# Kernel tuning notes

Hardware: AMD Instinct MI355X
Metric: run time of the kernel (lower is better)

The kernel has to match this reference:

```python
import jax, jax.numpy as jnp
import numpy as np

B, S, F, H, DK = 16, 1024, 512, 8, 64
NEG = 999999.0

def setup_inputs() -> dict:
    key = jax.random.key(0)
    ks = jax.random.split(key, 10)
    s = 1.0 / np.sqrt(F)
    inp = {
        'x': jax.random.normal(ks[0], (B, S, F), dtype=jnp.float32),
        'xlen': jax.random.randint(ks[1], (B,), 1, S + 1, dtype=jnp.int32),
        'WQw': jax.random.uniform(ks[2], (H, DK, F), jnp.float32, -s, s),
        'WQb': jax.random.uniform(ks[3], (H, DK), jnp.float32, -s, s),
        'WKw': jax.random.uniform(ks[4], (H, DK, F), jnp.float32, -s, s),
        'WKb': jax.random.uniform(ks[5], (H, DK), jnp.float32, -s, s),
        'WVw': jax.random.uniform(ks[6], (H, DK, F), jnp.float32, -s, s),
        'WVb': jax.random.uniform(ks[7], (H, DK), jnp.float32, -s, s),
        'WOw': jax.random.uniform(ks[8], (F, H * DK), jnp.float32, -1.0/np.sqrt(H*DK), 1.0/np.sqrt(H*DK)),
        'WOb': jax.random.uniform(ks[9], (F,), jnp.float32, -1.0/np.sqrt(H*DK), 1.0/np.sqrt(H*DK)),
    }
    return inp

def reference(x, xlen, WQw, WQb, WKw, WKb, WVw, WVb, WOw, WOb):
    # batched per-head projections: [B,S,F] x [H,DK,F] -> [B,H,S,DK]
    q = jnp.einsum('bsf,hdf->bhsd', x, WQw) + WQb[None, :, None, :]
    k = jnp.einsum('bsf,hdf->bhsd', x, WKw) + WKb[None, :, None, :]
    v = jnp.einsum('bsf,hdf->bhsd', x, WVw) + WVb[None, :, None, :]
    scores = jnp.einsum('bhsd,bhtd->bhst', q, k) / jnp.sqrt(jnp.float32(DK))
    # additive padding mask; original masks key positions >= xlen[j]-1 (off-by-one preserved)
    key_pos = jnp.arange(S)[None, :]                       # [1,S]
    mask = jnp.where(key_pos >= (xlen - 1)[:, None], -NEG, 0.0).astype(jnp.float32)
    scores = scores + mask[:, None, None, :]               # [B,H,S,S]
    attn = jax.nn.softmax(scores, axis=-1)
    z = jnp.einsum('bhst,bhtd->bhsd', attn, v)             # [B,H,S,DK]
    z = jnp.transpose(z, (0, 2, 1, 3)).reshape(B, S, H * DK)  # concat heads
    return z @ WOw.T + WOb
```

## Files before the change

### kernel.cpp

```cpp
#include <hip/hip_runtime.h>

typedef short bf16x8 __attribute__((ext_vector_type(8)));
typedef float f32x4 __attribute__((ext_vector_type(4)));
typedef unsigned short u16;

#define B_   16
#define S_   1024
#define F_   512
#define H_   8
#define DK_  64


__device__ __forceinline__ u16 f2bf(float f) {
    union { float f; unsigned int u; } v; v.f = f;
    return (u16)((v.u + 0x7FFFu + ((v.u >> 16) & 1u)) >> 16);
}
__device__ __forceinline__ float bf2f(u16 h) {
    union { unsigned int u; float f; } v; v.u = ((unsigned int)h) << 16;
    return v.f;
}
__device__ __forceinline__ bf16x8 cvt8(float4 a, float4 b) {
    union { u16 u[8]; bf16x8 v; } r;
    r.u[0] = f2bf(a.x); r.u[1] = f2bf(a.y); r.u[2] = f2bf(a.z); r.u[3] = f2bf(a.w);
    r.u[4] = f2bf(b.x); r.u[5] = f2bf(b.y); r.u[6] = f2bf(b.z); r.u[7] = f2bf(b.w);
    return r.v;
}

__device__ __forceinline__ void gl_lds16(const u16* g, u16* l) {
    __builtin_amdgcn_global_load_lds(
        (const __attribute__((address_space(1))) unsigned int*)g,
        (__attribute__((address_space(3))) unsigned int*)l,
        16, 0, 0);
}

__global__ __launch_bounds__(256) void cvt_all(
    const float* __restrict__ x,
    const float* __restrict__ wq, const float* __restrict__ wk,
    const float* __restrict__ wv, const float* __restrict__ wo,
    const float* __restrict__ bq, const float* __restrict__ bk,
    const float* __restrict__ bv, const float* __restrict__ bo,
    u16* __restrict__ Xbf, u16* __restrict__ Wbase)
{
    const size_t u = (size_t)blockIdx.x * 256 + threadIdx.x;
    const float* src; u16* dst;
    if (u < 1048576)      { src = x  + u * 8;               dst = Xbf + u * 8; }
    else if (u < 1081344) { src = wq + (u - 1048576) * 8;   dst = Wbase + (u - 1048576) * 8; }
    else if (u < 1114112) { src = wk + (u - 1081344) * 8;   dst = Wbase +  262144 + (u - 1081344) * 8; }
    else if (u < 1146880) { src = wv + (u - 1114112) * 8;   dst = Wbase +  524288 + (u - 1114112) * 8; }
    else if (u < 1179648) { src = wo + (u - 1146880) * 8;   dst = Wbase +  786432 + (u - 1146880) * 8; }
    else if (u < 1179712) { src = bq + (u - 1179648) * 8;   dst = Wbase + 1048576 + (u - 1179648) * 8; }
    else if (u < 1179776) { src = bk + (u - 1179712) * 8;   dst = Wbase + 1049088 + (u - 1179712) * 8; }
    else if (u < 1179840) { src = bv + (u - 1179776) * 8;   dst = Wbase + 1049600 + (u - 1179776) * 8; }
    else                  { src = bo + (u - 1179840) * 8;   dst = Wbase + 1050112 + (u - 1179840) * 8; }
    *(bf16x8*)dst = cvt8(*(const float4*)src, *(const float4*)(src + 4));
}

template <int EPI>
__global__ __launch_bounds__(256) void gemm128(
    const u16* __restrict__ A, const u16* __restrict__ Bm,
    const u16* __restrict__ bias, void* __restrict__ out)
{
    __shared__ __align__(16) u16 AsL[4096];
    __shared__ __align__(16) u16 BsL[4096];

    const int t    = threadIdx.x;
    const int wave = t >> 6, lane = t & 63;
    const int l15  = lane & 15, quad = lane >> 4;
    const int wr   = (wave & 1) * 64, wc = (wave >> 1) * 64;
    const int m0   = blockIdx.x * 128, n0 = blockIdx.y * 128;
    const int sr   = t >> 2, scol = (t & 3) * 8;

    f32x4 acc[4][4];
#pragma unroll
    for (int i = 0; i < 4; i++)
#pragma unroll
        for (int j = 0; j < 4; j++) acc[i][j] = {0.f, 0.f, 0.f, 0.f};

    const u16* Ab = A  + (size_t)(m0 + sr) * 512 + scol;
    const u16* Bb = Bm + (size_t)(n0 + sr) * 512 + scol;
    u16* la = &AsL[t * 8];
    u16* lb = &BsL[t * 8];

    for (int k0 = 0; k0 < 512; k0 += 32) {
        gl_lds16(Ab + k0,         la);
        gl_lds16(Ab + 32768 + k0, la + 2048);
        gl_lds16(Bb + k0,         lb);
        gl_lds16(Bb + 32768 + k0, lb + 2048);
        __syncthreads();
        bf16x8 af[4], bfv[4];
#pragma unroll
        for (int i = 0; i < 4; i++) af[i]  = *(const bf16x8*)&AsL[(wr + i * 16 + l15) * 32 + quad * 8];
#pragma unroll
        for (int j = 0; j < 4; j++) bfv[j] = *(const bf16x8*)&BsL[(wc + j * 16 + l15) * 32 + quad * 8];
#pragma unroll
        for (int i = 0; i < 4; i++)
#pragma unroll
            for (int j = 0; j < 4; j++)
                acc[i][j] = __builtin_amdgcn_mfma_f32_16x16x32_bf16(af[i], bfv[j], acc[i][j], 0, 0, 0);
        __syncthreads();
    }

#pragma unroll
    for (int j = 0; j < 4; j++) {
        const int n  = n0 + wc + j * 16 + l15;
        const float bv = bf2f(bias[n]);
        const int hh = n >> 6, d = n & 63;
#pragma unroll
        for (int i = 0; i < 4; i++) {
#pragma unroll
            for (int r = 0; r < 4; r++) {
                const int m = m0 + wr + i * 16 + quad * 4 + r;
                const float val = acc[i][j][r] + bv;
                if (EPI == 0) {
                    const int b = m >> 10, s = m & 1023;
                    ((u16*)out)[((size_t)(b * 8 + hh) * 1024 + s) * 64 + d] = f2bf(val);
                } else if (EPI == 1) {
                    const int b = m >> 10, s = m & 1023;
                    ((u16*)out)[((size_t)(b * 8 + hh) * 64 + d) * 1024 + s] = f2bf(val);
                } else {
                    ((float*)out)[(size_t)m * 512 + n] = val;
                }
            }
        }
    }
}

__global__ __launch_bounds__(256) void attn(
    const u16* __restrict__ Xbf, const u16* __restrict__ Wqbf,
    const u16* __restrict__ bqbf,
    const u16* __restrict__ Kg, const u16* __restrict__ Vt,
    const int* __restrict__ xlen, u16* __restrict__ Z)
{
    __shared__ __align__(16) u16 smem[13824];

    const int t    = threadIdx.x;
    const int wave = t >> 6, lane = t & 63;
    const int l15  = lane & 15, quad = lane >> 4;
    const int bh   = blockIdx.y, b = bh >> 3, h = bh & 7;
    const int bx   = blockIdx.x;
    const int xm1  = xlen[b] - 1;
    const int wm   = (wave & 1) * 32, wn = (wave >> 1) * 32;

    u16* Ks = smem;
    u16* Vs = smem + 4608;
    u16* PQ = smem + 9216 + wave * 1152;

    f32x4 qa[2][2];
#pragma unroll
    for (int i = 0; i < 2; i++)
#pragma unroll
        for (int j = 0; j < 2; j++) qa[i][j] = {0.f, 0.f, 0.f, 0.f};

    const int sr = t >> 2, scol = (t & 3) * 8;
    const u16* Xb = Xbf  + (size_t)(b * 1024 + bx * 64 + sr) * 512 + scol;
    const u16* Wb = Wqbf + (size_t)(h * 64 + sr) * 512 + scol;
    u16* la = &smem[t * 8];
    u16* lb = &smem[2048 + t * 8];

    for (int k0 = 0; k0 < 512; k0 += 32) {
        gl_lds16(Xb + k0, la);
        gl_lds16(Wb + k0, lb);
        __syncthreads();
        bf16x8 af[2], bfv[2];
#pragma unroll
        for (int i = 0; i < 2; i++) af[i]  = *(const bf16x8*)&smem[(wm + i * 16 + l15) * 32 + quad * 8];
#pragma unroll
        for (int j = 0; j < 2; j++) bfv[j] = *(const bf16x8*)&smem[2048 + (wn + j * 16 + l15) * 32 + quad * 8];
#pragma unroll
        for (int i = 0; i < 2; i++)
#pragma unroll
            for (int j = 0; j < 2; j++)
                qa[i][j] = __builtin_amdgcn_mfma_f32_16x16x32_bf16(af[i], bfv[j], qa[i][j], 0, 0, 0);
        __syncthreads();
    }
#pragma unroll
    for (int j = 0; j < 2; j++) {
        const int d  = wn + j * 16 + l15;
        const float bv = bf2f(bqbf[h * 64 + d]);
#pragma unroll
        for (int i = 0; i < 2; i++) {
#pragma unroll
            for (int r = 0; r < 4; r++) {
                const int row = wm + i * 16 + quad * 4 + r;
                smem[9216 + (row >> 4) * 1152 + (row & 15) * 72 + d] = f2bf((qa[i][j][r] + bv) * 0.125f);
            }
        }
    }
    __syncthreads();

    bf16x8 aq[2];
#pragma unroll
    for (int kk = 0; kk < 2; kk++)
        aq[kk] = *(const bf16x8*)&PQ[l15 * 72 + kk * 32 + quad * 8];

    const size_t baseKV = (size_t)bh * (S_ * DK_);
    const bool domask = (xm1 >= 1);
    const int  Slim   = domask ? xm1 : S_;

    f32x4 o[4];
#pragma unroll
    for (int j = 0; j < 4; j++) o[j] = {0.f, 0.f, 0.f, 0.f};
    float li[4] = {0.f, 0.f, 0.f, 0.f};

    const int srow = t >> 3, scl = (t & 7) * 8;

    for (int t0 = 0; t0 < Slim; t0 += 64) {
        *(uint4*)&Ks[srow * 72 + scl]        = *(const uint4*)&Kg[baseKV + (size_t)(t0 + srow) * 64 + scl];
        *(uint4*)&Ks[(srow + 32) * 72 + scl] = *(const uint4*)&Kg[baseKV + (size_t)(t0 + srow + 32) * 64 + scl];
        *(uint4*)&Vs[srow * 72 + scl]        = *(const uint4*)&Vt[baseKV + (size_t)srow * 1024 + t0 + scl];
        *(uint4*)&Vs[(srow + 32) * 72 + scl] = *(const uint4*)&Vt[baseKV + (size_t)(srow + 32) * 1024 + t0 + scl];
        __syncthreads();

        f32x4 sc[4];
#pragma unroll
        for (int nh = 0; nh < 4; nh++) {
            f32x4 s = {0.f, 0.f, 0.f, 0.f};
#pragma unroll
            for (int kk = 0; kk < 2; kk++) {
                bf16x8 bk = *(const bf16x8*)&Ks[(nh * 16 + l15) * 72 + kk * 32 + quad * 8];
                s = __builtin_amdgcn_mfma_f32_16x16x32_bf16(aq[kk], bk, s, 0, 0, 0);
            }
            sc[nh] = s;
        }
        if (domask && (t0 + 64 > xm1)) {
#pragma unroll
            for (int nh = 0; nh < 4; nh++) {
                const float madd = ((t0 + nh * 16 + l15) >= xm1) ? -999999.0f : 0.0f;
#pragma unroll
                for (int r = 0; r < 4; r++) sc[nh][r] += madd;
            }
        }
#pragma unroll
        for (int r = 0; r < 4; r++) {
            float e0 = __expf(sc[0][r]), e1 = __expf(sc[1][r]);
            float e2 = __expf(sc[2][r]), e3 = __expf(sc[3][r]);
            li[r] += (e0 + e1) + (e2 + e3);
            PQ[(quad * 4 + r) * 72 + l15]      = f2bf(e0);
            PQ[(quad * 4 + r) * 72 + 16 + l15] = f2bf(e1);
            PQ[(quad * 4 + r) * 72 + 32 + l15] = f2bf(e2);
            PQ[(quad * 4 + r) * 72 + 48 + l15] = f2bf(e3);
        }
        bf16x8 ap[2];
#pragma unroll
        for (int kk = 0; kk < 2; kk++)
            ap[kk] = *(const bf16x8*)&PQ[l15 * 72 + kk * 32 + quad * 8];
#pragma unroll
        for (int j = 0; j < 4; j++) {
#pragma unroll
            for (int kk = 0; kk < 2; kk++) {
                bf16x8 bv8 = *(const bf16x8*)&Vs[(j * 16 + l15) * 72 + kk * 32 + quad * 8];
                o[j] = __builtin_amdgcn_mfma_f32_16x16x32_bf16(ap[kk], bv8, o[j], 0, 0, 0);
            }
        }
        __syncthreads();
    }

    float linv[4];
#pragma unroll
    for (int r = 0; r < 4; r++) {
        float rs = li[r];
#pragma unroll
        for (int msk = 1; msk < 16; msk <<= 1) rs += __shfl_xor(rs, msk);
        linv[r] = 1.0f / rs;
    }
#pragma unroll
    for (int j = 0; j < 4; j++) {
#pragma unroll
        for (int r = 0; r < 4; r++) {
            const int s = bx * 64 + wave * 16 + quad * 4 + r;
            Z[((size_t)(b * 1024 + s)) * 512 + h * 64 + j * 16 + l15] = f2bf(o[j][r] * linv[r]);
        }
    }
}

extern "C" void kernel_launch(void* const* d_in, const int* in_sizes, int n_in,
                              void* d_out, int out_size, void* d_ws, size_t ws_size,
                              hipStream_t stream)
{
    (void)in_sizes; (void)n_in; (void)out_size; (void)ws_size;

    const float* x    = (const float*)d_in[0];
    const int*   xlen = (const int*)d_in[1];
    const float* WQw  = (const float*)d_in[2];
    const float* WQb  = (const float*)d_in[3];
    const float* WKw  = (const float*)d_in[4];
    const float* WKb  = (const float*)d_in[5];
    const float* WVw  = (const float*)d_in[6];
    const float* WVb  = (const float*)d_in[7];
    const float* WOw  = (const float*)d_in[8];
    const float* WOb  = (const float*)d_in[9];

    const size_t NQ = (size_t)B_ * H_ * S_ * DK_;
    u16* Kb    = (u16*)d_ws;
    u16* Zb    = Kb + NQ;
    u16* Wbase = Zb + NQ;
    u16* WQbf  = Wbase;
    u16* WKbf  = Wbase + 262144;
    u16* WVbf  = Wbase + 524288;
    u16* WObf  = Wbase + 786432;
    u16* bqbf  = Wbase + 1048576;
    u16* bkbf  = Wbase + 1049088;
    u16* bvbf  = Wbase + 1049600;
    u16* bobf  = Wbase + 1050112;
    u16* Xbf = (u16*)d_out;
    u16* Vb  = Xbf + NQ;

    dim3 blk(256);
    cvt_all<<<dim3(4609), blk, 0, stream>>>(x, WQw, WKw, WVw, WOw,
                                            WQb, WKb, WVb, WOb, Xbf, Wbase);

    dim3 gGemm(128, 4);
    gemm128<0><<<gGemm, blk, 0, stream>>>(Xbf, WKbf, bkbf, Kb);
    gemm128<1><<<gGemm, blk, 0, stream>>>(Xbf, WVbf, bvbf, Vb);

    dim3 gAttn(16, 128);
    attn<<<gAttn, blk, 0, stream>>>(Xbf, WQbf, bqbf, Kb, Vb, xlen, Zb);

    gemm128<2><<<gGemm, blk, 0, stream>>>(Zb, WObf, bobf, d_out);
}
```

Before: 212.4 us.

## Keep attention probabilities in registers by transposing QK^T and permuting K rows

The QK^T MFMA now runs with operands swapped (K as A, Q as B), so each lane holds scores along the key dimension. K rows are stored in LDS with a permutation, which lets the exponentiated scores be packed directly into bf16 A-operand fragments for the PV MFMA. This removes the per-tile LDS write and read of P along with its buffer, and it changes the mask index math and the row-sum reduction to match. The smaller LDS footprint and the launch-bounds hint of 8 blocks aim to raise occupancy, but the register limit may cause spills.

After: 233.9 us. +10.1%, slower.

```diff
diff --git a/kernel.cpp b/kernel.cpp
--- a/kernel.cpp
+++ b/kernel.cpp
@@ -1,4 +1,5 @@
 #include <hip/hip_runtime.h>
+#include <hip/hip_bf16.h>
 
 typedef short bf16x8 __attribute__((ext_vector_type(8)));
 typedef float f32x4 __attribute__((ext_vector_type(4)));
@@ -24,6 +25,11 @@
     r.u[0] = f2bf(a.x); r.u[1] = f2bf(a.y); r.u[2] = f2bf(a.z); r.u[3] = f2bf(a.w);
     r.u[4] = f2bf(b.x); r.u[5] = f2bf(b.y); r.u[6] = f2bf(b.z); r.u[7] = f2bf(b.w);
     return r.v;
+}
+__device__ __forceinline__ unsigned int pk2(float lo, float hi) {
+    union { __hip_bfloat162 h; unsigned int u; } c;
+    c.h = __float22bfloat162_rn(make_float2(lo, hi));
+    return c.u;
 }
 
 __device__ __forceinline__ void gl_lds16(const u16* g, u16* l) {
@@ -125,13 +131,13 @@
     }
 }
 
-__global__ __launch_bounds__(256) void attn(
+__global__ __launch_bounds__(256, 8) void attn(
     const u16* __restrict__ Xbf, const u16* __restrict__ Wqbf,
     const u16* __restrict__ bqbf,
     const u16* __restrict__ Kg, const u16* __restrict__ Vt,
     const int* __restrict__ xlen, u16* __restrict__ Z)
 {
-    __shared__ __align__(16) u16 smem[13824];
+    __shared__ __align__(16) u16 smem[9216];
 
     const int t    = threadIdx.x;
     const int wave = t >> 6, lane = t & 63;
@@ -143,7 +149,6 @@
 
     u16* Ks = smem;
     u16* Vs = smem + 4608;
-    u16* PQ = smem + 9216 + wave * 1152;
 
     f32x4 qa[2][2];
 #pragma unroll
@@ -182,7 +187,7 @@
 #pragma unroll
             for (int r = 0; r < 4; r++) {
                 const int row = wm + i * 16 + quad * 4 + r;
-                smem[9216 + (row >> 4) * 1152 + (row & 15) * 72 + d] = f2bf((qa[i][j][r] + bv) * 0.125f);
+                smem[row * 72 + d] = f2bf((qa[i][j][r] + bv) * 0.125f);
             }
         }
     }
@@ -191,7 +196,8 @@
     bf16x8 aq[2];
 #pragma unroll
     for (int kk = 0; kk < 2; kk++)
-        aq[kk] = *(const bf16x8*)&PQ[l15 * 72 + kk * 32 + quad * 8];
+        aq[kk] = *(const bf16x8*)&smem[(wave * 16 + l15) * 72 + kk * 32 + quad * 8];
+    __syncthreads();
 
     const size_t baseKV = (size_t)bh * (S_ * DK_);
     const bool domask = (xm1 >= 1);
@@ -200,13 +206,14 @@
     f32x4 o[4];
 #pragma unroll
     for (int j = 0; j < 4; j++) o[j] = {0.f, 0.f, 0.f, 0.f};
-    float li[4] = {0.f, 0.f, 0.f, 0.f};
+    float li = 0.f;
 
     const int srow = t >> 3, scl = (t & 7) * 8;
+    const int prow = ((srow >> 2) & 1) * 16 + (srow >> 3) * 4 + (srow & 3);
 
     for (int t0 = 0; t0 < Slim; t0 += 64) {
-        *(uint4*)&Ks[srow * 72 + scl]        = *(const uint4*)&Kg[baseKV + (size_t)(t0 + srow) * 64 + scl];
-        *(uint4*)&Ks[(srow + 32) * 72 + scl] = *(const uint4*)&Kg[baseKV + (size_t)(t0 + srow + 32) * 64 + scl];
+        *(uint4*)&Ks[prow * 72 + scl]        = *(const uint4*)&Kg[baseKV + (size_t)(t0 + srow) * 64 + scl];
+        *(uint4*)&Ks[(prow + 32) * 72 + scl] = *(const uint4*)&Kg[baseKV + (size_t)(t0 + srow + 32) * 64 + scl];
         *(uint4*)&Vs[srow * 72 + scl]        = *(const uint4*)&Vt[baseKV + (size_t)srow * 1024 + t0 + scl];
         *(uint4*)&Vs[(srow + 32) * 72 + scl] = *(const uint4*)&Vt[baseKV + (size_t)(srow + 32) * 1024 + t0 + scl];
         __syncthreads();
@@ -218,57 +225,54 @@
 #pragma unroll
             for (int kk = 0; kk < 2; kk++) {
                 bf16x8 bk = *(const bf16x8*)&Ks[(nh * 16 + l15) * 72 + kk * 32 + quad * 8];
-                s = __builtin_amdgcn_mfma_f32_16x16x32_bf16(aq[kk], bk, s, 0, 0, 0);
+                s = __builtin_amdgcn_mfma_f32_16x16x32_bf16(bk, aq[kk], s, 0, 0, 0);
             }
             sc[nh] = s;
         }
         if (domask && (t0 + 64 > xm1)) {
 #pragma unroll
             for (int nh = 0; nh < 4; nh++) {
-                const float madd = ((t0 + nh * 16 + l15) >= xm1) ? -999999.0f : 0.0f;
-#pragma unroll
-                for (int r = 0; r < 4; r++) sc[nh][r] += madd;
+                const int kb = t0 + ((nh >> 1) << 5) + (quad << 3) + ((nh & 1) << 2);
+#pragma unroll
+                for (int r = 0; r < 4; r++)
+                    sc[nh][r] += ((kb + r) >= xm1) ? -999999.0f : 0.0f;
             }
         }
 #pragma unroll
-        for (int r = 0; r < 4; r++) {
-            float e0 = __expf(sc[0][r]), e1 = __expf(sc[1][r]);
-            float e2 = __expf(sc[2][r]), e3 = __expf(sc[3][r]);
-            li[r] += (e0 + e1) + (e2 + e3);
-            PQ[(quad * 4 + r) * 72 + l15]      = f2bf(e0);
-            PQ[(quad * 4 + r) * 72 + 16 + l15] = f2bf(e1);
-            PQ[(quad * 4 + r) * 72 + 32 + l15] = f2bf(e2);
-            PQ[(quad * 4 + r) * 72 + 48 + l15] = f2bf(e3);
-        }
-        bf16x8 ap[2];
-#pragma unroll
-        for (int kk = 0; kk < 2; kk++)
-            ap[kk] = *(const bf16x8*)&PQ[l15 * 72 + kk * 32 + quad * 8];
+        for (int nh = 0; nh < 4; nh++) {
+#pragma unroll
+            for (int r = 0; r < 4; r++) sc[nh][r] = __expf(sc[nh][r]);
+            li += (sc[nh][0] + sc[nh][1]) + (sc[nh][2] + sc[nh][3]);
+        }
+        union { unsigned int u[4]; bf16x8 v; } ap0, ap1;
+        ap0.u[0] = pk2(sc[0][0], sc[0][1]); ap0.u[1] = pk2(sc[0][2], sc[0][3]);
+        ap0.u[2] = pk2(sc[1][0], sc[1][1]); ap0.u[3] = pk2(sc[1][2], sc[1][3]);
+        ap1.u[0] = pk2(sc[2][0], sc[2][1]); ap1.u[1] = pk2(sc[2][2], sc[2][3]);
+        ap1.u[2] = pk2(sc[3][0], sc[3][1]); ap1.u[3] = pk2(sc[3][2], sc[3][3]);
 #pragma unroll
         for (int j = 0; j < 4; j++) {
-#pragma unroll
-            for (int kk = 0; kk < 2; kk++) {
-                bf16x8 bv8 = *(const bf16x8*)&Vs[(j * 16 + l15) * 72 + kk * 32 + quad * 8];
-                o[j] = __builtin_amdgcn_mfma_f32_16x16x32_bf16(ap[kk], bv8, o[j], 0, 0, 0);
-            }
-        }
-        __syncthreads();
-    }
-
-    float linv[4];
-#pragma unroll
-    for (int r = 0; r < 4; r++) {
-        float rs = li[r];
-#pragma unroll
-        for (int msk = 1; msk < 16; msk <<= 1) rs += __shfl_xor(rs, msk);
-        linv[r] = 1.0f / rs;
-    }
+            bf16x8 bv0 = *(const bf16x8*)&Vs[(j * 16 + l15) * 72 + quad * 8];
+            o[j] = __builtin_amdgcn_mfma_f32_16x16x32_bf16(ap0.v, bv0, o[j], 0, 0, 0);
+            bf16x8 bv1 = *(const bf16x8*)&Vs[(j * 16 + l15) * 72 + 32 + quad * 8];
+            o[j] = __builtin_amdgcn_mfma_f32_16x16x32_bf16(ap1.v, bv1, o[j], 0, 0, 0);
+        }
+        __syncthreads();
+    }
+
+    float rs = li;
+    rs += __shfl_xor(rs, 16);
+    rs += __shfl_xor(rs, 32);
+    const float linv = 1.0f / rs;
+    float lr[4];
+#pragma unroll
+    for (int r = 0; r < 4; r++) lr[r] = __shfl(linv, quad * 4 + r);
+
 #pragma unroll
     for (int j = 0; j < 4; j++) {
 #pragma unroll
         for (int r = 0; r < 4; r++) {
             const int s = bx * 64 + wave * 16 + quad * 4 + r;
-            Z[((size_t)(b * 1024 + s)) * 512 + h * 64 + j * 16 + l15] = f2bf(o[j][r] * linv[r]);
+            Z[((size_t)(b * 1024 + s)) * 512 + h * 64 + j * 16 + l15] = f2bf(o[j][r] * lr[r]);
         }
     }
 }
```
